# Kernel optimization log

Measured on AMD Instinct MI355X. Metric: run time of the kernel, lower is better.

Reference implementation:

```python
import jax, jax.numpy as jnp
import numpy as np

N = 100000
IN_CH = 128
OUT_CH = 32
HEADS = 4
E = 1600000
NEG_SLOPE = 0.2  # PyG GATConv default negative_slope


def setup_inputs() -> dict:
    key = jax.random.key(0)
    k_x, k_e, k_w, k_as, k_ad, k_b = jax.random.split(key, 6)
    x = jax.random.normal(k_x, (N, IN_CH), dtype=jnp.float32)
    edge_index = jax.random.randint(k_e, (2, E), 0, N, dtype=jnp.int64)
    # Glorot-style scale for linear weight, small normals for attention vectors
    W = jax.random.normal(k_w, (IN_CH, HEADS * OUT_CH), dtype=jnp.float32) * (1.0 / np.sqrt(IN_CH))
    att_src = jax.random.normal(k_as, (1, HEADS, OUT_CH), dtype=jnp.float32) * 0.1
    att_dst = jax.random.normal(k_ad, (1, HEADS, OUT_CH), dtype=jnp.float32) * 0.1
    bias = jnp.zeros((HEADS * OUT_CH,), dtype=jnp.float32)
    return {"x": x, "edge_index": edge_index, "W": W,
            "att_src": att_src, "att_dst": att_dst, "bias": bias}


def reference(x, edge_index, W, att_src, att_dst, bias):
    n = x.shape[0]
    # Linear transform: [N, H, C]
    xw = (x @ W).reshape(n, HEADS, OUT_CH)
    # Per-node attention logits: [N, H]
    a_src = (xw * att_src).sum(-1)
    a_dst = (xw * att_dst).sum(-1)
    # Add self-loops (PyG GATConv default add_self_loops=True)
    loop = jnp.arange(n, dtype=edge_index.dtype)
    src = jnp.concatenate([edge_index[0], loop])  # [E']
    dst = jnp.concatenate([edge_index[1], loop])  # [E']
    # Edge-wise attention logits + leaky relu: [E', H]
    alpha = jax.nn.leaky_relu(a_src[src] + a_dst[dst], NEG_SLOPE)
    # Segment softmax over edges grouped by destination node
    amax = jax.ops.segment_max(alpha, dst, num_segments=n)
    alpha = jnp.exp(alpha - amax[dst])
    denom = jax.ops.segment_sum(alpha, dst, num_segments=n)
    alpha = alpha / (denom[dst] + 1e-16)
    # Weighted scatter-aggregate of source features: [N, H, C]
    msg = xw[src] * alpha[:, :, None]
    out = jax.ops.segment_sum(msg, dst, num_segments=n)
    out = out.reshape(n, HEADS * OUT_CH) + bias
    return jax.nn.elu(out)
```

## Files before the change

kernel.cpp:

```cpp
#include <hip/hip_runtime.h>
#include <cmath>


#define LOG2E 1.44269504088896340736f

typedef float f32x2 __attribute__((ext_vector_type(2)));
typedef float f32x4 __attribute__((ext_vector_type(4)));
typedef unsigned u32x4 __attribute__((ext_vector_type(4)));
typedef short bf16x8 __attribute__((ext_vector_type(8)));

__device__ __forceinline__ float fast_exp2(float x) {
#if __has_builtin(__builtin_amdgcn_exp2f)
  return __builtin_amdgcn_exp2f(x);
#else
  return exp2f(x);
#endif
}

__device__ __forceinline__ unsigned bf16_rne(float f) {
  unsigned u = __float_as_uint(f);
  return (u + 0x7fffu + ((u >> 16) & 1u)) >> 16;
}
__device__ __forceinline__ float bf_lo(unsigned v) {
  return __uint_as_float(v << 16);
}
__device__ __forceinline__ float bf_hi(unsigned v) {
  return __uint_as_float(v & 0xffff0000u);
}

__device__ __forceinline__ int blockInclScan(int v, int tid, int* lds) {
  int lane = tid & 63;
  int wid = tid >> 6;
#pragma unroll
  for (int off = 1; off < 64; off <<= 1) {
    int t = __shfl_up(v, off);
    if (lane >= off) v += t;
  }
  if (lane == 63) lds[wid] = v;
  __syncthreads();
  int add = 0;
  for (int i = 0; i < wid; ++i) add += lds[i];
  v += add;
  __syncthreads();
  return v;
}

#define CHUNK 4096
#define MAXE 2560

__global__ __launch_bounds__(256) void k_hist(const int* __restrict__ ei, int E,
                                              int EL, int NB2, int NBLK,
                                              int* __restrict__ bh,
                                              int* __restrict__ btot,
                                              const float* __restrict__ Wm,
                                              const float* __restrict__ att_src,
                                              const float* __restrict__ att_dst,
                                              unsigned short* __restrict__ u_bf) {
  if ((int)blockIdx.x == NBLK) {
    int k = threadIdx.x;
    if (k < 128) {
      const float* wr = Wm + (size_t)k * 128;
      float s[8] = {0.f, 0.f, 0.f, 0.f, 0.f, 0.f, 0.f, 0.f};
      for (int c = 0; c < 32; ++c) {
#pragma unroll
        for (int h = 0; h < 4; ++h) {
          float wv = wr[h * 32 + c];
          s[h] = fmaf(wv, att_src[h * 32 + c], s[h]);
          s[4 + h] = fmaf(wv, att_dst[h * 32 + c], s[4 + h]);
        }
      }
#pragma unroll
      for (int j = 0; j < 8; ++j)
        u_bf[k * 8 + j] = (unsigned short)bf16_rne(s[j]);
    }
    return;
  }
  __shared__ int lh[1792];
  int tid = threadIdx.x;
  for (int b = tid; b < NB2; b += 256) lh[b] = 0;
  __syncthreads();
  int base_e = blockIdx.x * CHUNK;
#pragma unroll
  for (int j = 0; j < CHUNK / 256; ++j) {
    int e = base_e + j * 256 + tid;
    if (e < EL) {
      int dst = (e < E) ? ei[E + e] : (e - E);
      atomicAdd(&lh[dst >> 6], 1);
    }
  }
  __syncthreads();
  for (int b = tid; b < NB2; b += 256) {
    int c = lh[b];
    bh[(size_t)b * NBLK + blockIdx.x] = c;
    if (c) atomicAdd(&btot[b], c);
  }
}

__global__ __launch_bounds__(256) void p2c_brow(int* __restrict__ bh,
                                                const int* __restrict__ btot,
                                                int* __restrict__ bbase,
                                                int NB2, int NBLK) {
  __shared__ int lds[4];
  __shared__ int ctot;
  __shared__ int red[256];
  int b = blockIdx.x;
  int tid = threadIdx.x;
  int part = 0;
  for (int j = tid; j < b; j += 256) part += btot[j];
  red[tid] = part;
  __syncthreads();
  for (int st = 128; st > 0; st >>= 1) {
    if (tid < st) red[tid] += red[tid + st];
    __syncthreads();
  }
  int base = red[0];
  if (tid == 0) bbase[b] = base;
  __syncthreads();
  int v0 = (tid < NBLK) ? bh[(size_t)b * NBLK + tid] : 0;
  int incl0 = blockInclScan(v0, tid, lds);
  if (tid < NBLK) bh[(size_t)b * NBLK + tid] = base + incl0 - v0;
  if (tid == 255) ctot = incl0;
  __syncthreads();
  int base1 = base + ctot;
  int j = 256 + tid;
  int v1 = (j < NBLK) ? bh[(size_t)b * NBLK + j] : 0;
  int incl1 = blockInclScan(v1, tid, lds);
  if (j < NBLK) bh[(size_t)b * NBLK + j] = base1 + incl1 - v1;
}

__global__ __launch_bounds__(256) void k_fusedB(
    const float* __restrict__ x, const float* __restrict__ Wm,
    const unsigned short* __restrict__ u_bf, unsigned* __restrict__ xwb,
    float* __restrict__ a_src, float* __restrict__ a_dst, int N, int GB2,
    const int* __restrict__ ei, int E, int EL, int NB2, int NBLK,
    const int* __restrict__ bh, unsigned* __restrict__ tmp) {
  __shared__ __align__(16) char sm[36864];
  const int tid = threadIdx.x;

  if ((int)blockIdx.x >= GB2) {
    int blk = blockIdx.x - GB2;
    int* lc = (int*)sm;
    for (int b = tid; b < NB2; b += 256) lc[b] = bh[(size_t)b * NBLK + blk];
    __syncthreads();
    int base_e = blk * CHUNK;
#pragma unroll
    for (int j = 0; j < CHUNK / 256; ++j) {
      int e = base_e + j * 256 + tid;
      if (e < EL) {
        int src, dst;
        if (e < E) {
          src = ei[e];
          dst = ei[E + e];
        } else {
          src = e - E;
          dst = e - E;
        }
        int pos = atomicAdd(&lc[dst >> 6], 1);
        tmp[pos] = ((unsigned)(dst & 63) << 17) | (unsigned)src;
      }
    }
    return;
  }

  short* Ws = (short*)sm;
  {
    int r = tid & 127;
    int ch = tid >> 7;
    int kk = r >> 5, g = (r >> 3) & 3, i = r & 7;
    short* drow = Ws + ((kk * 4 + g) * 144) * 8 + i;
    const float* srow = Wm + (size_t)r * 128 + ch * 64;
#pragma unroll
    for (int c4 = 0; c4 < 16; ++c4) {
      float4 v = *(const float4*)&srow[c4 * 4];
      int c0 = ch * 64 + c4 * 4;
      drow[(c0 + 0) * 8] = (short)bf16_rne(v.x);
      drow[(c0 + 1) * 8] = (short)bf16_rne(v.y);
      drow[(c0 + 2) * 8] = (short)bf16_rne(v.z);
      drow[(c0 + 3) * 8] = (short)bf16_rne(v.w);
    }
    if (tid < 128) {
#pragma unroll
      for (int j = 0; j < 8; ++j) drow[(128 + j) * 8] = (short)u_bf[r * 8 + j];
#pragma unroll
      for (int j = 8; j < 16; ++j) drow[(128 + j) * 8] = 0;
    }
  }
  __syncthreads();

  const int w = tid >> 6;
  const int l = tid & 63;
  const int lr = l & 15;
  const int lg = l >> 4;
  const int row0w = blockIdx.x * 64 + w * 16;
  const int arow = row0w + lr;

  f32x4 acc[9];
#pragma unroll
  for (int t = 0; t < 9; ++t) acc[t] = (f32x4){0.f, 0.f, 0.f, 0.f};

  const float* xrow = x + (size_t)arow * 128 + lg * 8;
#pragma unroll
  for (int kk = 0; kk < 4; ++kk) {
    unsigned p0 = 0, p1 = 0, p2 = 0, p3 = 0;
    if (arow < N) {
      float4 f0 = *(const float4*)&xrow[kk * 32];
      float4 f1 = *(const float4*)&xrow[kk * 32 + 4];
      p0 = bf16_rne(f0.x) | (bf16_rne(f0.y) << 16);
      p1 = bf16_rne(f0.z) | (bf16_rne(f0.w) << 16);
      p2 = bf16_rne(f1.x) | (bf16_rne(f1.y) << 16);
      p3 = bf16_rne(f1.z) | (bf16_rne(f1.w) << 16);
    }
    u32x4 ap = {p0, p1, p2, p3};
    bf16x8 af = __builtin_bit_cast(bf16x8, ap);
    const short* wsbase = Ws + ((kk * 4 + lg) * 144 + lr) * 8;
#pragma unroll
    for (int t = 0; t < 9; ++t) {
      bf16x8 bf = *(const bf16x8*)(wsbase + t * 128);
      acc[t] = __builtin_amdgcn_mfma_f32_16x16x32_bf16(af, bf, acc[t], 0, 0, 0);
    }
  }

#pragma unroll
  for (int t = 0; t < 8; ++t) {
#pragma unroll
    for (int i = 0; i < 4; ++i) {
      float v = acc[t][i];
      float vn = __shfl_xor(v, 1);
      int row = row0w + 4 * lg + i;
      if (!(l & 1) && row < N) {
        unsigned pk = bf16_rne(v) | (bf16_rne(vn) << 16);
        xwb[(size_t)row * 64 + 8 * t + (lr >> 1)] = pk;
      }
    }
  }
#pragma unroll
  for (int i = 0; i < 4; ++i) {
    int row = row0w + 4 * lg + i;
    if (lr < 8 && row < N) {
      float v = acc[8][i] * LOG2E;
      if (lr < 4) a_src[row * 4 + lr] = v;
      else a_dst[row * 4 + lr - 4] = v;
    }
  }
}

__global__ __launch_bounds__(256) void k_bagg(
    const unsigned* __restrict__ tmp, const int* __restrict__ bbase,
    const int* __restrict__ btot, const float* __restrict__ asrc,
    const float* __restrict__ adst, const unsigned* __restrict__ xwb,
    const float* __restrict__ bias, float* __restrict__ out, int N) {
  __shared__ unsigned sorted[MAXE];
  __shared__ int deg[64];
  __shared__ int startd[64];
  __shared__ int cur[64];
  const int bid = blockIdx.x;
  const int tid = threadIdx.x;
  const int beg = bbase[bid];
  const int cnt = btot[bid];
  if (tid < 64) deg[tid] = 0;
  __syncthreads();
  for (int k = tid; k < cnt; k += 256) {
    unsigned w = tmp[beg + k];
    atomicAdd(&deg[w >> 17], 1);
  }
  __syncthreads();
  if (tid < 64) {
    int v = deg[tid];
    int incl = v;
#pragma unroll
    for (int off = 1; off < 64; off <<= 1) {
      int t = __shfl_up(incl, off);
      if (tid >= off) incl += t;
    }
    int excl = incl - v;
    startd[tid] = excl;
    cur[tid] = excl;
  }
  __syncthreads();
  for (int k = tid; k < cnt; k += 256) {
    unsigned w = tmp[beg + k];
    int pos = atomicAdd(&cur[w >> 17], 1);
    if (pos < MAXE) sorted[pos] = w;
  }
  __syncthreads();
  const int wv = tid >> 6;
  const int lane = tid & 63;
  const int half = lane >> 5;
  const int l5 = lane & 31;
  const int h = l5 >> 3;
  const unsigned* xr = xwb + l5 * 2;
  const float4 bv = *(const float4*)&bias[l5 * 4];

  for (int j = 0; j < 16; ++j) {
    int dl = wv + 4 * j;
    int gdst = bid * 64 + dl;
    if (gdst >= N) break;
    int sd = startd[dl];
    int ed = min(sd + deg[dl], MAXE);
    float ad = adst[gdst * 4 + h];

    float sA = 0.f, sB = 0.f;
    float a0 = 0.f, a1 = 0.f, a2 = 0.f, a3 = 0.f;
    float b0 = 0.f, b1 = 0.f, b2 = 0.f, b3 = 0.f;
    int i = sd + half;
    for (; i + 6 < ed; i += 8) {
      unsigned wA = sorted[i], wB = sorted[i + 2];
      unsigned wC = sorted[i + 4], wD = sorted[i + 6];
      int eA = wA & 0x1FFFF, eB = wB & 0x1FFFF;
      int eC = wC & 0x1FFFF, eD = wD & 0x1FFFF;
      float tA = asrc[eA * 4 + h] + ad;
      float tB = asrc[eB * 4 + h] + ad;
      float tC = asrc[eC * 4 + h] + ad;
      float tD = asrc[eD * 4 + h] + ad;
      uint2 vA = *(const uint2*)(xr + (size_t)eA * 64);
      uint2 vB = *(const uint2*)(xr + (size_t)eB * 64);
      uint2 vC = *(const uint2*)(xr + (size_t)eC * 64);
      uint2 vD = *(const uint2*)(xr + (size_t)eD * 64);
      float pA = fast_exp2(fmaxf(tA, 0.2f * tA));
      float pB = fast_exp2(fmaxf(tB, 0.2f * tB));
      float pC = fast_exp2(fmaxf(tC, 0.2f * tC));
      float pD = fast_exp2(fmaxf(tD, 0.2f * tD));
      sA += pA + pC;
      sB += pB + pD;
      a0 = fmaf(pA, bf_lo(vA.x), a0);
      a1 = fmaf(pA, bf_hi(vA.x), a1);
      a2 = fmaf(pA, bf_lo(vA.y), a2);
      a3 = fmaf(pA, bf_hi(vA.y), a3);
      b0 = fmaf(pB, bf_lo(vB.x), b0);
      b1 = fmaf(pB, bf_hi(vB.x), b1);
      b2 = fmaf(pB, bf_lo(vB.y), b2);
      b3 = fmaf(pB, bf_hi(vB.y), b3);
      a0 = fmaf(pC, bf_lo(vC.x), a0);
      a1 = fmaf(pC, bf_hi(vC.x), a1);
      a2 = fmaf(pC, bf_lo(vC.y), a2);
      a3 = fmaf(pC, bf_hi(vC.y), a3);
      b0 = fmaf(pD, bf_lo(vD.x), b0);
      b1 = fmaf(pD, bf_hi(vD.x), b1);
      b2 = fmaf(pD, bf_lo(vD.y), b2);
      b3 = fmaf(pD, bf_hi(vD.y), b3);
    }
    for (; i < ed; i += 2) {
      unsigned wA = sorted[i];
      int eA = wA & 0x1FFFF;
      float tA = asrc[eA * 4 + h] + ad;
      uint2 vA = *(const uint2*)(xr + (size_t)eA * 64);
      float pA = fast_exp2(fmaxf(tA, 0.2f * tA));
      sA += pA;
      a0 = fmaf(pA, bf_lo(vA.x), a0);
      a1 = fmaf(pA, bf_hi(vA.x), a1);
      a2 = fmaf(pA, bf_lo(vA.y), a2);
      a3 = fmaf(pA, bf_hi(vA.y), a3);
    }
    float s = sA + sB;
    a0 += b0;
    a1 += b1;
    a2 += b2;
    a3 += b3;
    s += __shfl_xor(s, 32);
    a0 += __shfl_xor(a0, 32);
    a1 += __shfl_xor(a1, 32);
    a2 += __shfl_xor(a2, 32);
    a3 += __shfl_xor(a3, 32);

    if (half == 0) {
      float inv = 1.f / s;
      float o0 = fmaf(a0, inv, bv.x);
      float o1 = fmaf(a1, inv, bv.y);
      float o2 = fmaf(a2, inv, bv.z);
      float o3 = fmaf(a3, inv, bv.w);
      o0 = o0 > 0.f ? o0 : fast_exp2(o0 * LOG2E) - 1.f;
      o1 = o1 > 0.f ? o1 : fast_exp2(o1 * LOG2E) - 1.f;
      o2 = o2 > 0.f ? o2 : fast_exp2(o2 * LOG2E) - 1.f;
      o3 = o3 > 0.f ? o3 : fast_exp2(o3 * LOG2E) - 1.f;
      f32x4 o = {o0, o1, o2, o3};
      __builtin_nontemporal_store(o, (f32x4*)&out[(size_t)gdst * 128 + l5 * 4]);
    }
  }
}

extern "C" void kernel_launch(void* const* d_in, const int* in_sizes, int n_in,
                              void* d_out, int out_size, void* d_ws, size_t ws_size,
                              hipStream_t stream) {
  const float* x = (const float*)d_in[0];
  const int* ei = (const int*)d_in[1];
  const float* Wm = (const float*)d_in[2];
  const float* att_src = (const float*)d_in[3];
  const float* att_dst = (const float*)d_in[4];
  const float* bias = (const float*)d_in[5];
  float* out = (float*)d_out;

  const int N = in_sizes[0] / 128;
  const int E = in_sizes[1] / 2;
  const int EL = E + N;
  const int NB2 = (N + 63) >> 6;
  const int NBLK = (EL + CHUNK - 1) / CHUNK;
  const int GB2 = (N + 63) / 64;

  size_t off = 0;
  auto carve = [&](size_t bytes) -> void* {
    void* p = (char*)d_ws + off;
    off += (bytes + 255) & ~(size_t)255;
    return p;
  };
  unsigned* xwb = (unsigned*)carve((size_t)N * 64 * 4);
  float* a_src = (float*)carve((size_t)N * 4 * 4);
  float* a_dst = (float*)carve((size_t)N * 4 * 4);
  unsigned* tmp = (unsigned*)carve((size_t)EL * 4);
  int* bh = (int*)carve((size_t)NB2 * NBLK * 4);
  int* btot = (int*)carve((size_t)NB2 * 4);
  int* bbase = (int*)carve((size_t)NB2 * 4);
  unsigned short* u_bf = (unsigned short*)carve(128 * 8 * 2);

  (void)hipMemsetAsync(btot, 0, (size_t)NB2 * 4, stream);

  k_hist<<<NBLK + 1, 256, 0, stream>>>(ei, E, EL, NB2, NBLK, bh, btot, Wm,
                                       att_src, att_dst, u_bf);
  p2c_brow<<<NB2, 256, 0, stream>>>(bh, btot, bbase, NB2, NBLK);
  k_fusedB<<<GB2 + NBLK, 256, 0, stream>>>(x, Wm, u_bf, xwb, a_src, a_dst, N,
                                           GB2, ei, E, EL, NB2, NBLK, bh, tmp);
  k_bagg<<<NB2, 256, 0, stream>>>(tmp, bbase, btot, a_src, a_dst, xwb,
                                  bias, out, N);
}
```

Measured before the change: 164.1 us.

## Widen fused GEMM blocks to 512 threads and use half-wave per destination node

k_fusedB now runs 512 threads per block. Each GEMM block covers 256 rows in two passes, so the bf16 weight tile staged in LDS is reused across four times as many rows. The edge-scatter part handles a chunk with half as many iterations per thread. In k_bagg each 32-lane half-wave now owns its own destination node instead of two halves splitting one node's edges, which removes the cross-half shuffle reduction but gives each lane more serial edges and leaves half-waves unevenly loaded when degrees differ.

```diff
diff --git a/kernel.cpp b/kernel.cpp
--- a/kernel.cpp
+++ b/kernel.cpp
@@ -128,7 +128,7 @@
   if (j < NBLK) bh[(size_t)b * NBLK + j] = base1 + incl1 - v1;
 }
 
-__global__ __launch_bounds__(256) void k_fusedB(
+__global__ __launch_bounds__(512) void k_fusedB(
     const float* __restrict__ x, const float* __restrict__ Wm,
     const unsigned short* __restrict__ u_bf, unsigned* __restrict__ xwb,
     float* __restrict__ a_src, float* __restrict__ a_dst, int N, int GB2,
@@ -140,12 +140,12 @@
   if ((int)blockIdx.x >= GB2) {
     int blk = blockIdx.x - GB2;
     int* lc = (int*)sm;
-    for (int b = tid; b < NB2; b += 256) lc[b] = bh[(size_t)b * NBLK + blk];
+    for (int b = tid; b < NB2; b += 512) lc[b] = bh[(size_t)b * NBLK + blk];
     __syncthreads();
     int base_e = blk * CHUNK;
 #pragma unroll
-    for (int j = 0; j < CHUNK / 256; ++j) {
-      int e = base_e + j * 256 + tid;
+    for (int j = 0; j < CHUNK / 512; ++j) {
+      int e = base_e + j * 512 + tid;
       if (e < EL) {
         int src, dst;
         if (e < E) {
@@ -165,14 +165,14 @@
   short* Ws = (short*)sm;
   {
     int r = tid & 127;
-    int ch = tid >> 7;
+    int q = tid >> 7;
     int kk = r >> 5, g = (r >> 3) & 3, i = r & 7;
     short* drow = Ws + ((kk * 4 + g) * 144) * 8 + i;
-    const float* srow = Wm + (size_t)r * 128 + ch * 64;
-#pragma unroll
-    for (int c4 = 0; c4 < 16; ++c4) {
+    const float* srow = Wm + (size_t)r * 128 + q * 32;
+#pragma unroll
+    for (int c4 = 0; c4 < 8; ++c4) {
       float4 v = *(const float4*)&srow[c4 * 4];
-      int c0 = ch * 64 + c4 * 4;
+      int c0 = q * 32 + c4 * 4;
       drow[(c0 + 0) * 8] = (short)bf16_rne(v.x);
       drow[(c0 + 1) * 8] = (short)bf16_rne(v.y);
       drow[(c0 + 2) * 8] = (short)bf16_rne(v.z);
@@ -191,55 +191,60 @@
   const int l = tid & 63;
   const int lr = l & 15;
   const int lg = l >> 4;
-  const int row0w = blockIdx.x * 64 + w * 16;
-  const int arow = row0w + lr;
-
-  f32x4 acc[9];
-#pragma unroll
-  for (int t = 0; t < 9; ++t) acc[t] = (f32x4){0.f, 0.f, 0.f, 0.f};
-
-  const float* xrow = x + (size_t)arow * 128 + lg * 8;
-#pragma unroll
-  for (int kk = 0; kk < 4; ++kk) {
-    unsigned p0 = 0, p1 = 0, p2 = 0, p3 = 0;
-    if (arow < N) {
-      float4 f0 = *(const float4*)&xrow[kk * 32];
-      float4 f1 = *(const float4*)&xrow[kk * 32 + 4];
-      p0 = bf16_rne(f0.x) | (bf16_rne(f0.y) << 16);
-      p1 = bf16_rne(f0.z) | (bf16_rne(f0.w) << 16);
-      p2 = bf16_rne(f1.x) | (bf16_rne(f1.y) << 16);
-      p3 = bf16_rne(f1.z) | (bf16_rne(f1.w) << 16);
-    }
-    u32x4 ap = {p0, p1, p2, p3};
-    bf16x8 af = __builtin_bit_cast(bf16x8, ap);
-    const short* wsbase = Ws + ((kk * 4 + lg) * 144 + lr) * 8;
-#pragma unroll
-    for (int t = 0; t < 9; ++t) {
-      bf16x8 bf = *(const bf16x8*)(wsbase + t * 128);
-      acc[t] = __builtin_amdgcn_mfma_f32_16x16x32_bf16(af, bf, acc[t], 0, 0, 0);
-    }
-  }
-
-#pragma unroll
-  for (int t = 0; t < 8; ++t) {
+
+#pragma unroll
+  for (int p = 0; p < 2; ++p) {
+    const int row0w = blockIdx.x * 256 + p * 128 + w * 16;
+    const int arow = row0w + lr;
+
+    f32x4 acc[9];
+#pragma unroll
+    for (int t = 0; t < 9; ++t) acc[t] = (f32x4){0.f, 0.f, 0.f, 0.f};
+
+    const float* xrow = x + (size_t)arow * 128 + lg * 8;
+#pragma unroll
+    for (int kk = 0; kk < 4; ++kk) {
+      unsigned p0 = 0, p1 = 0, p2 = 0, p3 = 0;
+      if (arow < N) {
+        float4 f0 = *(const float4*)&xrow[kk * 32];
+        float4 f1 = *(const float4*)&xrow[kk * 32 + 4];
+        p0 = bf16_rne(f0.x) | (bf16_rne(f0.y) << 16);
+        p1 = bf16_rne(f0.z) | (bf16_rne(f0.w) << 16);
+        p2 = bf16_rne(f1.x) | (bf16_rne(f1.y) << 16);
+        p3 = bf16_rne(f1.z) | (bf16_rne(f1.w) << 16);
+      }
+      u32x4 ap = {p0, p1, p2, p3};
+      bf16x8 af = __builtin_bit_cast(bf16x8, ap);
+      const short* wsbase = Ws + ((kk * 4 + lg) * 144 + lr) * 8;
+#pragma unroll
+      for (int t = 0; t < 9; ++t) {
+        bf16x8 bf = *(const bf16x8*)(wsbase + t * 128);
+        acc[t] =
+            __builtin_amdgcn_mfma_f32_16x16x32_bf16(af, bf, acc[t], 0, 0, 0);
+      }
+    }
+
+#pragma unroll
+    for (int t = 0; t < 8; ++t) {
+#pragma unroll
+      for (int i = 0; i < 4; ++i) {
+        float v = acc[t][i];
+        float vn = __shfl_xor(v, 1);
+        int row = row0w + 4 * lg + i;
+        if (!(l & 1) && row < N) {
+          unsigned pk = bf16_rne(v) | (bf16_rne(vn) << 16);
+          xwb[(size_t)row * 64 + 8 * t + (lr >> 1)] = pk;
+        }
+      }
+    }
 #pragma unroll
     for (int i = 0; i < 4; ++i) {
-      float v = acc[t][i];
-      float vn = __shfl_xor(v, 1);
       int row = row0w + 4 * lg + i;
-      if (!(l & 1) && row < N) {
-        unsigned pk = bf16_rne(v) | (bf16_rne(vn) << 16);
-        xwb[(size_t)row * 64 + 8 * t + (lr >> 1)] = pk;
-      }
-    }
-  }
-#pragma unroll
-  for (int i = 0; i < 4; ++i) {
-    int row = row0w + 4 * lg + i;
-    if (lr < 8 && row < N) {
-      float v = acc[8][i] * LOG2E;
-      if (lr < 4) a_src[row * 4 + lr] = v;
-      else a_dst[row * 4 + lr - 4] = v;
+      if (lr < 8 && row < N) {
+        float v = acc[8][i] * LOG2E;
+        if (lr < 4) a_src[row * 4 + lr] = v;
+        else a_dst[row * 4 + lr - 4] = v;
+      }
     }
   }
 }
@@ -285,27 +290,29 @@
   __syncthreads();
   const int wv = tid >> 6;
   const int lane = tid & 63;
-  const int half = lane >> 5;
+  const int hf = lane >> 5;
   const int l5 = lane & 31;
   const int h = l5 >> 3;
+  const int slot = wv * 2 + hf;
   const unsigned* xr = xwb + l5 * 2;
   const float4 bv = *(const float4*)&bias[l5 * 4];
 
-  for (int j = 0; j < 16; ++j) {
-    int dl = wv + 4 * j;
+#pragma unroll
+  for (int j = 0; j < 8; ++j) {
+    int dl = slot + 8 * j;
     int gdst = bid * 64 + dl;
-    if (gdst >= N) break;
-    int sd = startd[dl];
-    int ed = min(sd + deg[dl], MAXE);
-    float ad = adst[gdst * 4 + h];
+    bool act = gdst < N;
+    int sd = act ? startd[dl] : 0;
+    int ed = act ? min(sd + deg[dl], MAXE) : 0;
+    float ad = act ? adst[gdst * 4 + h] : 0.f;
 
     float sA = 0.f, sB = 0.f;
     float a0 = 0.f, a1 = 0.f, a2 = 0.f, a3 = 0.f;
     float b0 = 0.f, b1 = 0.f, b2 = 0.f, b3 = 0.f;
-    int i = sd + half;
-    for (; i + 6 < ed; i += 8) {
-      unsigned wA = sorted[i], wB = sorted[i + 2];
-      unsigned wC = sorted[i + 4], wD = sorted[i + 6];
+    int i = sd;
+    for (; i + 3 < ed; i += 4) {
+      unsigned wA = sorted[i], wB = sorted[i + 1];
+      unsigned wC = sorted[i + 2], wD = sorted[i + 3];
       int eA = wA & 0x1FFFF, eB = wB & 0x1FFFF;
       int eC = wC & 0x1FFFF, eD = wD & 0x1FFFF;
       float tA = asrc[eA * 4 + h] + ad;
@@ -339,7 +346,7 @@
       b2 = fmaf(pD, bf_lo(vD.y), b2);
       b3 = fmaf(pD, bf_hi(vD.y), b3);
     }
-    for (; i < ed; i += 2) {
+    for (; i < ed; ++i) {
       unsigned wA = sorted[i];
       int eA = wA & 0x1FFFF;
       float tA = asrc[eA * 4 + h] + ad;
@@ -351,23 +358,12 @@
       a2 = fmaf(pA, bf_lo(vA.y), a2);
       a3 = fmaf(pA, bf_hi(vA.y), a3);
     }
-    float s = sA + sB;
-    a0 += b0;
-    a1 += b1;
-    a2 += b2;
-    a3 += b3;
-    s += __shfl_xor(s, 32);
-    a0 += __shfl_xor(a0, 32);
-    a1 += __shfl_xor(a1, 32);
-    a2 += __shfl_xor(a2, 32);
-    a3 += __shfl_xor(a3, 32);
-
-    if (half == 0) {
-      float inv = 1.f / s;
-      float o0 = fmaf(a0, inv, bv.x);
-      float o1 = fmaf(a1, inv, bv.y);
-      float o2 = fmaf(a2, inv, bv.z);
-      float o3 = fmaf(a3, inv, bv.w);
+    if (act) {
+      float inv = 1.f / (sA + sB);
+      float o0 = fmaf(a0 + b0, inv, bv.x);
+      float o1 = fmaf(a1 + b1, inv, bv.y);
+      float o2 = fmaf(a2 + b2, inv, bv.z);
+      float o3 = fmaf(a3 + b3, inv, bv.w);
       o0 = o0 > 0.f ? o0 : fast_exp2(o0 * LOG2E) - 1.f;
       o1 = o1 > 0.f ? o1 : fast_exp2(o1 * LOG2E) - 1.f;
       o2 = o2 > 0.f ? o2 : fast_exp2(o2 * LOG2E) - 1.f;
@@ -394,7 +390,7 @@
   const int EL = E + N;
   const int NB2 = (N + 63) >> 6;
   const int NBLK = (EL + CHUNK - 1) / CHUNK;
-  const int GB2 = (N + 63) / 64;
+  const int GB2 = (N + 255) / 256;
 
   size_t off = 0;
   auto carve = [&](size_t bytes) -> void* {
@@ -416,7 +412,7 @@
   k_hist<<<NBLK + 1, 256, 0, stream>>>(ei, E, EL, NB2, NBLK, bh, btot, Wm,
                                        att_src, att_dst, u_bf);
   p2c_brow<<<NB2, 256, 0, stream>>>(bh, btot, bbase, NB2, NBLK);
-  k_fusedB<<<GB2 + NBLK, 256, 0, stream>>>(x, Wm, u_bf, xwb, a_src, a_dst, N,
+  k_fusedB<<<GB2 + NBLK, 512, 0, stream>>>(x, Wm, u_bf, xwb, a_src, a_dst, N,
                                            GB2, ei, E, EL, NB2, NBLK, bh, tmp);
   k_bagg<<<NB2, 256, 0, stream>>>(tmp, bbase, btot, a_src, a_dst, xwb,
                                   bias, out, N);
```

After: 160.6 us. 1.02x faster.
